# Optimization experiments

Hardware: AMD Instinct MI355X
Metric: run time of the kernel (lower is better)

Reference implementation:

```python
import jax, jax.numpy as jnp
import numpy as np

N_QUBITS = 8
EMBED_DIM = 1024
FFN_DIM = 4096


def _apply_1q_batched(state, gate, wire):
    # state: [N] + [2]*n ; gate: [N,2,2] (per-sample)
    n = state.ndim - 1
    N = state.shape[0]
    L = 2 ** wire
    R = 2 ** (n - 1 - wire)
    st = state.reshape(N, L, 2, R)
    st = jnp.einsum('nba,nlar->nlbr', gate, st)
    return st.reshape((N,) + (2,) * n)


def _apply_1q_shared(state, gate, wire):
    # gate: [2,2] shared across samples
    n = state.ndim - 1
    N = state.shape[0]
    L = 2 ** wire
    R = 2 ** (n - 1 - wire)
    st = state.reshape(N, L, 2, R)
    st = jnp.einsum('ba,nlar->nlbr', gate, st)
    return st.reshape((N,) + (2,) * n)


def _cnot(state, control, target):
    c_ax = control + 1
    t_ax = target + 1
    s0 = jnp.take(state, 0, axis=c_ax)
    s1 = jnp.take(state, 1, axis=c_ax)
    t_ax2 = t_ax - 1 if t_ax > c_ax else t_ax  # axis shift after take
    s1 = jnp.flip(s1, axis=t_ax2)
    return jnp.stack([s0, s1], axis=c_ax)


def _simulate(q_inputs, qparams):
    # q_inputs: [N, n_qubits] RX angles; qparams: [n_qubits, 3] Rot(phi,theta,omega)
    N = q_inputs.shape[0]
    n = N_QUBITS
    state = jnp.zeros((N, 2 ** n), dtype=jnp.complex64).at[:, 0].set(1.0)
    state = state.reshape((N,) + (2,) * n)
    # RX layer (per-sample angles)
    half = q_inputs.astype(jnp.float32) * 0.5
    c = jnp.cos(half).astype(jnp.complex64)
    s = (-1j) * jnp.sin(half).astype(jnp.complex64)
    for i in range(n):
        gate = jnp.stack([jnp.stack([c[:, i], s[:, i]], -1),
                          jnp.stack([s[:, i], c[:, i]], -1)], -2)  # [N,2,2]
        state = _apply_1q_batched(state, gate, i)
    # Rot layer: Rot(phi, theta, omega) = RZ(omega) RY(theta) RZ(phi)
    for i in range(n):
        phi, theta, omega = qparams[i, 0], qparams[i, 1], qparams[i, 2]
        ct = jnp.cos(theta / 2).astype(jnp.complex64)
        st = jnp.sin(theta / 2).astype(jnp.complex64)
        ep = jnp.exp(-0.5j * (phi + omega).astype(jnp.complex64))
        em = jnp.exp(0.5j * (phi - omega).astype(jnp.complex64))
        gate = jnp.array(0., jnp.complex64) + jnp.stack([
            jnp.stack([ep * ct, -em * st]),
            jnp.stack([jnp.conj(em) * st, jnp.conj(ep) * ct])])
        state = _apply_1q_shared(state, gate, i)
    # CNOT ring
    for i in range(n - 1):
        state = _cnot(state, i, i + 1)
    state = _cnot(state, n - 1, 0)
    # PauliZ expectations
    probs = jnp.abs(state) ** 2  # [N] + [2]*n, float32
    zs = []
    for i in range(n):
        axes = tuple(a for a in range(1, n + 1) if a != i + 1)
        m = probs.sum(axes)  # [N,2]
        zs.append(m[:, 0] - m[:, 1])
    return jnp.stack(zs, -1)  # [N, n_qubits]


def setup_inputs() -> dict:
    key = jax.random.key(0)
    k = jax.random.split(key, 6)
    x = jax.random.normal(k[0], (4, 2048, EMBED_DIM), dtype=jnp.float32)
    W1 = jax.random.normal(k[1], (FFN_DIM, EMBED_DIM), dtype=jnp.float32) * 0.02
    b1 = jnp.zeros((FFN_DIM,), dtype=jnp.float32)
    qparams = jax.random.normal(k[2], (N_QUBITS, 3), dtype=jnp.float32)
    W2 = jax.random.normal(k[3], (EMBED_DIM, N_QUBITS), dtype=jnp.float32) * 0.02
    b2 = jnp.zeros((EMBED_DIM,), dtype=jnp.float32)
    return {"x": x, "W1": W1, "b1": b1, "qparams": qparams, "W2": W2, "b2": b2}


def reference(x, W1, b1, qparams, W2, b2):
    batch, seq_len, embed_dim = x.shape
    x_flat = x.reshape(-1, embed_dim)
    x_ffn = x_flat @ W1.T + b1                       # [N, ffn_dim]
    q_inputs = x_ffn[:, :N_QUBITS]                   # ffn_dim >= n_qubits
    q_out = _simulate(q_inputs, qparams)             # [N, n_qubits]
    out = q_out @ W2.T + b2                          # [N, embed_dim]
    return out.reshape(batch, seq_len, embed_dim)
```

## Files before the change

kernel.cpp:

```cpp
#include <hip/hip_runtime.h>
#include <math.h>


constexpr int EMBED = 1024;
constexpr int NQ    = 8;
constexpr int BLOCK = 256;
constexpr int RPW   = 4;
constexpr int BR    = 16;
constexpr float INV2PI = 0.15915494309189535f;

__global__ __launch_bounds__(BLOCK, 2)
void ffq(const float* __restrict__ x,
         const float* __restrict__ W1,
         const float* __restrict__ b1,
         const float* __restrict__ qp,
         const float* __restrict__ W2,
         const float* __restrict__ b2,
         float* __restrict__ out,
         int total_rows)
{
    const int t    = threadIdx.x;
    const int lane = t & 63;
    const int wv   = t >> 6;
    const int j    = lane & 7;

    __shared__ float w1s[NQ * EMBED];
    __shared__ float w2t[NQ * EMBED];

    const long r0 = (long)blockIdx.x * BR + wv * RPW;

    float4 xv[RPW][4];
#pragma unroll
    for (int r = 0; r < RPW; ++r) {
        long row = r0 + r; if (row >= total_rows) row = total_rows - 1;
#pragma unroll
        for (int i = 0; i < 4; ++i)
            xv[r][i] = *reinterpret_cast<const float4*>(
                x + (size_t)row * EMBED + i * 256 + lane * 4);
    }

    {
        const float4* w1g = reinterpret_cast<const float4*>(W1);
        float4* w1d = reinterpret_cast<float4*>(w1s);
#pragma unroll
        for (int k = 0; k < (NQ * EMBED / 4) / BLOCK; ++k)
            w1d[k * BLOCK + t] = w1g[k * BLOCK + t];
#pragma unroll
        for (int m = 0; m < 4; ++m) {
            const int col = m * BLOCK + t;
            const float4 a = *reinterpret_cast<const float4*>(W2 + col * NQ);
            const float4 b = *reinterpret_cast<const float4*>(W2 + col * NQ + 4);
            w2t[0 * EMBED + col] = a.x;  w2t[1 * EMBED + col] = a.y;
            w2t[2 * EMBED + col] = a.z;  w2t[3 * EMBED + col] = a.w;
            w2t[4 * EMBED + col] = b.x;  w2t[5 * EMBED + col] = b.y;
            w2t[6 * EMBED + col] = b.z;  w2t[7 * EMBED + col] = b.w;
        }
    }

    float Rj, qoffj;
    {
        const float phi  = qp[j * 3 + 0];
        const float th   = qp[j * 3 + 1];
        const float cth  = cosf(th);
        const float ssps = sinf(th) * sinf(phi);
        Rj    = sqrtf(cth * cth + ssps * ssps);
        qoffj = (b1[j] + atan2f(ssps, cth)) * INV2PI;
    }

    float4 b2v[4];
#pragma unroll
    for (int i = 0; i < 4; ++i)
        b2v[i] = *reinterpret_cast<const float4*>(b2 + i * 256 + lane * 4);

    __syncthreads();

    float p[RPW][NQ];
#pragma unroll
    for (int r = 0; r < RPW; ++r)
#pragma unroll
        for (int jj = 0; jj < NQ; ++jj) p[r][jj] = 0.f;

#pragma unroll
    for (int i = 0; i < 4; ++i) {
#pragma unroll
        for (int jj = 0; jj < NQ; ++jj) {
            const float4 w = *reinterpret_cast<const float4*>(
                w1s + jj * EMBED + i * 256 + lane * 4);
#pragma unroll
            for (int r = 0; r < RPW; ++r) {
                p[r][jj] = fmaf(xv[r][i].x, w.x, p[r][jj]);
                p[r][jj] = fmaf(xv[r][i].y, w.y, p[r][jj]);
                p[r][jj] = fmaf(xv[r][i].z, w.z, p[r][jj]);
                p[r][jj] = fmaf(xv[r][i].w, w.w, p[r][jj]);
            }
        }
    }

    float qo[RPW][NQ];
#pragma unroll
    for (int r = 0; r < RPW; ++r) {
        float q4[4], q2[2], tsum;
        {
            const bool up = (lane & 4);
#pragma unroll
            for (int k = 0; k < 4; ++k) {
                const float snd = up ? p[r][k]     : p[r][k + 4];
                const float kp  = up ? p[r][k + 4] : p[r][k];
                q4[k] = kp + __shfl_xor(snd, 4, 64);
            }
        }
        {
            const bool up = (lane & 2);
#pragma unroll
            for (int k = 0; k < 2; ++k) {
                const float snd = up ? q4[k]     : q4[k + 2];
                const float kp  = up ? q4[k + 2] : q4[k];
                q2[k] = kp + __shfl_xor(snd, 2, 64);
            }
        }
        {
            const bool up = (lane & 1);
            const float snd = up ? q2[0] : q2[1];
            const float kp  = up ? q2[1] : q2[0];
            tsum = kp + __shfl_xor(snd, 1, 64);
        }
        tsum += __shfl_xor(tsum, 8, 64);
        tsum += __shfl_xor(tsum, 16, 64);
        tsum += __shfl_xor(tsum, 32, 64);

        const float zz = Rj * __builtin_amdgcn_cosf(tsum * INV2PI + qoffj);

        float z0_, z1_, z2_, z3_, z4_, z5_, z6_, z7_;
        {
            const float o  = __shfl_xor(zz, 1, 64);
            const float a0 = (lane & 1) ? o  : zz;
            const float a1 = (lane & 1) ? zz : o;
            const float rA = __shfl_xor(a0, 2, 64);
            const float rB = __shfl_xor(a1, 2, 64);
            const float c0 = (lane & 2) ? rA : a0;
            const float c1 = (lane & 2) ? rB : a1;
            const float c2 = (lane & 2) ? a0 : rA;
            const float c3 = (lane & 2) ? a1 : rB;
            const float d0 = __shfl_xor(c0, 4, 64);
            const float d1 = __shfl_xor(c1, 4, 64);
            const float d2 = __shfl_xor(c2, 4, 64);
            const float d3 = __shfl_xor(c3, 4, 64);
            z0_ = (lane & 4) ? d0 : c0;
            z1_ = (lane & 4) ? d1 : c1;
            z2_ = (lane & 4) ? d2 : c2;
            z3_ = (lane & 4) ? d3 : c3;
            z4_ = (lane & 4) ? c0 : d0;
            z5_ = (lane & 4) ? c1 : d1;
            z6_ = (lane & 4) ? c2 : d2;
            z7_ = (lane & 4) ? c3 : d3;
        }

        qo[r][1] = z0_ * z1_;
        qo[r][2] = qo[r][1] * z2_;
        qo[r][3] = qo[r][2] * z3_;
        qo[r][4] = qo[r][3] * z4_;
        qo[r][5] = qo[r][4] * z5_;
        qo[r][6] = qo[r][5] * z6_;
        qo[r][7] = qo[r][6] * z7_;
        qo[r][0] = z1_ * z2_ * z3_ * z4_ * z5_ * z6_ * z7_;
    }

#pragma unroll
    for (int i = 0; i < 4; ++i) {
        float4 w[NQ];
#pragma unroll
        for (int jj = 0; jj < NQ; ++jj)
            w[jj] = *reinterpret_cast<const float4*>(
                w2t + jj * EMBED + i * 256 + lane * 4);

#pragma unroll
        for (int r = 0; r < RPW; ++r) {
            const long row = r0 + r;
            if (row >= total_rows) continue;
            float4 o = b2v[i];
#pragma unroll
            for (int jj = 0; jj < NQ; ++jj) {
                o.x = fmaf(qo[r][jj], w[jj].x, o.x);
                o.y = fmaf(qo[r][jj], w[jj].y, o.y);
                o.z = fmaf(qo[r][jj], w[jj].z, o.z);
                o.w = fmaf(qo[r][jj], w[jj].w, o.w);
            }
            *reinterpret_cast<float4*>(
                out + (size_t)row * EMBED + i * 256 + lane * 4) = o;
        }
    }
}

extern "C" void kernel_launch(void* const* d_in, const int* in_sizes, int n_in,
                              void* d_out, int out_size, void* d_ws, size_t ws_size,
                              hipStream_t stream) {
    const float* x  = (const float*)d_in[0];
    const float* W1 = (const float*)d_in[1];
    const float* b1 = (const float*)d_in[2];
    const float* qp = (const float*)d_in[3];
    const float* W2 = (const float*)d_in[4];
    const float* b2 = (const float*)d_in[5];
    float* out = (float*)d_out;

    const int rows = in_sizes[0] / EMBED;
    const int grid = (rows + BR - 1) / BR;

    hipLaunchKernelGGL(ffq, dim3(grid), dim3(BLOCK), 0, stream,
                       x, W1, b1, qp, W2, b2, out, rows);
}
```

Before: 102.0 us.

## Keep W2 slice in registers and share qubit outputs via LDS across block rows

```diff
diff --git a/kernel.cpp b/kernel.cpp
--- a/kernel.cpp
+++ b/kernel.cpp
@@ -5,11 +5,11 @@
 constexpr int EMBED = 1024;
 constexpr int NQ    = 8;
 constexpr int BLOCK = 256;
-constexpr int RPW   = 4;
-constexpr int BR    = 16;
+constexpr int RPW   = 2;
+constexpr int BR    = 8;
 constexpr float INV2PI = 0.15915494309189535f;
 
-__global__ __launch_bounds__(BLOCK, 2)
+__global__ __launch_bounds__(BLOCK, 3)
 void ffq(const float* __restrict__ x,
          const float* __restrict__ W1,
          const float* __restrict__ b1,
@@ -25,37 +25,29 @@
     const int j    = lane & 7;
 
     __shared__ float w1s[NQ * EMBED];
-    __shared__ float w2t[NQ * EMBED];
-
-    const long r0 = (long)blockIdx.x * BR + wv * RPW;
+    __shared__ float qoS[BR][NQ];
+
+    const long blk0 = (long)blockIdx.x * BR;
+    const long r0w  = blk0 + wv * RPW;
 
     float4 xv[RPW][4];
 #pragma unroll
     for (int r = 0; r < RPW; ++r) {
-        long row = r0 + r; if (row >= total_rows) row = total_rows - 1;
+        long row = r0w + r; if (row >= total_rows) row = total_rows - 1;
 #pragma unroll
         for (int i = 0; i < 4; ++i)
             xv[r][i] = *reinterpret_cast<const float4*>(
                 x + (size_t)row * EMBED + i * 256 + lane * 4);
     }
 
-    {
-        const float4* w1g = reinterpret_cast<const float4*>(W1);
-        float4* w1d = reinterpret_cast<float4*>(w1s);
-#pragma unroll
-        for (int k = 0; k < (NQ * EMBED / 4) / BLOCK; ++k)
-            w1d[k * BLOCK + t] = w1g[k * BLOCK + t];
-#pragma unroll
-        for (int m = 0; m < 4; ++m) {
-            const int col = m * BLOCK + t;
-            const float4 a = *reinterpret_cast<const float4*>(W2 + col * NQ);
-            const float4 b = *reinterpret_cast<const float4*>(W2 + col * NQ + 4);
-            w2t[0 * EMBED + col] = a.x;  w2t[1 * EMBED + col] = a.y;
-            w2t[2 * EMBED + col] = a.z;  w2t[3 * EMBED + col] = a.w;
-            w2t[4 * EMBED + col] = b.x;  w2t[5 * EMBED + col] = b.y;
-            w2t[6 * EMBED + col] = b.z;  w2t[7 * EMBED + col] = b.w;
-        }
-    }
+    const int c = wv * 256 + lane * 4;
+    float4 wA[4], wB[4];
+#pragma unroll
+    for (int q = 0; q < 4; ++q) {
+        wA[q] = *reinterpret_cast<const float4*>(W2 + (c + q) * NQ);
+        wB[q] = *reinterpret_cast<const float4*>(W2 + (c + q) * NQ + 4);
+    }
+    const float4 bb = *reinterpret_cast<const float4*>(b2 + c);
 
     float Rj, qoffj;
     {
@@ -67,10 +59,13 @@
         qoffj = (b1[j] + atan2f(ssps, cth)) * INV2PI;
     }
 
-    float4 b2v[4];
-#pragma unroll
-    for (int i = 0; i < 4; ++i)
-        b2v[i] = *reinterpret_cast<const float4*>(b2 + i * 256 + lane * 4);
+    {
+        const float4* w1g = reinterpret_cast<const float4*>(W1);
+        float4* w1d = reinterpret_cast<float4*>(w1s);
+#pragma unroll
+        for (int k = 0; k < (NQ * EMBED / 4) / BLOCK; ++k)
+            w1d[k * BLOCK + t] = w1g[k * BLOCK + t];
+    }
 
     __syncthreads();
 
@@ -96,7 +91,6 @@
         }
     }
 
-    float qo[RPW][NQ];
 #pragma unroll
     for (int r = 0; r < RPW; ++r) {
         float q4[4], q2[2], tsum;
@@ -155,39 +149,49 @@
             z7_ = (lane & 4) ? c3 : d3;
         }
 
-        qo[r][1] = z0_ * z1_;
-        qo[r][2] = qo[r][1] * z2_;
-        qo[r][3] = qo[r][2] * z3_;
-        qo[r][4] = qo[r][3] * z4_;
-        qo[r][5] = qo[r][4] * z5_;
-        qo[r][6] = qo[r][5] * z6_;
-        qo[r][7] = qo[r][6] * z7_;
-        qo[r][0] = z1_ * z2_ * z3_ * z4_ * z5_ * z6_ * z7_;
-    }
-
-#pragma unroll
-    for (int i = 0; i < 4; ++i) {
-        float4 w[NQ];
-#pragma unroll
-        for (int jj = 0; jj < NQ; ++jj)
-            w[jj] = *reinterpret_cast<const float4*>(
-                w2t + jj * EMBED + i * 256 + lane * 4);
-
-#pragma unroll
-        for (int r = 0; r < RPW; ++r) {
-            const long row = r0 + r;
-            if (row >= total_rows) continue;
-            float4 o = b2v[i];
-#pragma unroll
-            for (int jj = 0; jj < NQ; ++jj) {
-                o.x = fmaf(qo[r][jj], w[jj].x, o.x);
-                o.y = fmaf(qo[r][jj], w[jj].y, o.y);
-                o.z = fmaf(qo[r][jj], w[jj].z, o.z);
-                o.w = fmaf(qo[r][jj], w[jj].w, o.w);
-            }
-            *reinterpret_cast<float4*>(
-                out + (size_t)row * EMBED + i * 256 + lane * 4) = o;
-        }
+        const float p1 = z0_ * z1_;
+        const float p2 = p1 * z2_;
+        const float p3 = p2 * z3_;
+        const float p4 = p3 * z4_;
+        const float p5 = p4 * z5_;
+        const float p6 = p5 * z6_;
+        const float p7 = p6 * z7_;
+        const float t7 = z1_ * z2_ * z3_ * z4_ * z5_ * z6_ * z7_;
+
+        float sel = p1;
+        sel = (j == 0) ? t7 : sel;
+        sel = (j == 2) ? p2 : sel;
+        sel = (j == 3) ? p3 : sel;
+        sel = (j == 4) ? p4 : sel;
+        sel = (j == 5) ? p5 : sel;
+        sel = (j == 6) ? p6 : sel;
+        sel = (j == 7) ? p7 : sel;
+
+        if (lane < NQ)
+            qoS[wv * RPW + r][lane] = sel;
+    }
+
+    __syncthreads();
+
+#pragma unroll
+    for (int r = 0; r < BR; ++r) {
+        const long row = blk0 + r;
+        if (row >= total_rows) break;
+
+        const float4 qA = *reinterpret_cast<const float4*>(&qoS[r][0]);
+        const float4 qB = *reinterpret_cast<const float4*>(&qoS[r][4]);
+
+        float4 o;
+        o.x = bb.x + qA.x*wA[0].x + qA.y*wA[0].y + qA.z*wA[0].z + qA.w*wA[0].w
+                   + qB.x*wB[0].x + qB.y*wB[0].y + qB.z*wB[0].z + qB.w*wB[0].w;
+        o.y = bb.y + qA.x*wA[1].x + qA.y*wA[1].y + qA.z*wA[1].z + qA.w*wA[1].w
+                   + qB.x*wB[1].x + qB.y*wB[1].y + qB.z*wB[1].z + qB.w*wB[1].w;
+        o.z = bb.z + qA.x*wA[2].x + qA.y*wA[2].y + qA.z*wA[2].z + qA.w*wA[2].w
+                   + qB.x*wB[2].x + qB.y*wB[2].y + qB.z*wB[2].z + qB.w*wB[2].w;
+        o.w = bb.w + qA.x*wA[3].x + qA.y*wA[3].y + qA.z*wA[3].z + qA.w*wA[3].w
+                   + qB.x*wB[3].x + qB.y*wB[3].y + qB.z*wB[3].z + qB.w*wB[3].w;
+
+        *reinterpret_cast<float4*>(out + (size_t)row * EMBED + c) = o;
     }
 }
 
```

After: 129.5 us. +27.0%, slower.

## Drop W2 LDS transpose, read W2 from global, halve rows per block, nontemporal stores

Applied to the files above, without the earlier changes.

```diff
diff --git a/kernel.cpp b/kernel.cpp
--- a/kernel.cpp
+++ b/kernel.cpp
@@ -5,11 +5,13 @@
 constexpr int EMBED = 1024;
 constexpr int NQ    = 8;
 constexpr int BLOCK = 256;
-constexpr int RPW   = 4;
-constexpr int BR    = 16;
+constexpr int RPW   = 2;
+constexpr int BR    = 8;
 constexpr float INV2PI = 0.15915494309189535f;
 
-__global__ __launch_bounds__(BLOCK, 2)
+using v4f = __attribute__((ext_vector_type(4))) float;
+
+__global__ __launch_bounds__(BLOCK, 3)
 void ffq(const float* __restrict__ x,
          const float* __restrict__ W1,
          const float* __restrict__ b1,
@@ -25,36 +27,18 @@
     const int j    = lane & 7;
 
     __shared__ float w1s[NQ * EMBED];
-    __shared__ float w2t[NQ * EMBED];
-
-    const long r0 = (long)blockIdx.x * BR + wv * RPW;
+
+    const long blk0 = (long)blockIdx.x * BR;
+    const long r0w  = blk0 + wv * RPW;
 
     float4 xv[RPW][4];
 #pragma unroll
     for (int r = 0; r < RPW; ++r) {
-        long row = r0 + r; if (row >= total_rows) row = total_rows - 1;
+        long row = r0w + r; if (row >= total_rows) row = total_rows - 1;
 #pragma unroll
         for (int i = 0; i < 4; ++i)
             xv[r][i] = *reinterpret_cast<const float4*>(
                 x + (size_t)row * EMBED + i * 256 + lane * 4);
-    }
-
-    {
-        const float4* w1g = reinterpret_cast<const float4*>(W1);
-        float4* w1d = reinterpret_cast<float4*>(w1s);
-#pragma unroll
-        for (int k = 0; k < (NQ * EMBED / 4) / BLOCK; ++k)
-            w1d[k * BLOCK + t] = w1g[k * BLOCK + t];
-#pragma unroll
-        for (int m = 0; m < 4; ++m) {
-            const int col = m * BLOCK + t;
-            const float4 a = *reinterpret_cast<const float4*>(W2 + col * NQ);
-            const float4 b = *reinterpret_cast<const float4*>(W2 + col * NQ + 4);
-            w2t[0 * EMBED + col] = a.x;  w2t[1 * EMBED + col] = a.y;
-            w2t[2 * EMBED + col] = a.z;  w2t[3 * EMBED + col] = a.w;
-            w2t[4 * EMBED + col] = b.x;  w2t[5 * EMBED + col] = b.y;
-            w2t[6 * EMBED + col] = b.z;  w2t[7 * EMBED + col] = b.w;
-        }
     }
 
     float Rj, qoffj;
@@ -67,10 +51,13 @@
         qoffj = (b1[j] + atan2f(ssps, cth)) * INV2PI;
     }
 
-    float4 b2v[4];
-#pragma unroll
-    for (int i = 0; i < 4; ++i)
-        b2v[i] = *reinterpret_cast<const float4*>(b2 + i * 256 + lane * 4);
+    {
+        const float4* w1g = reinterpret_cast<const float4*>(W1);
+        float4* w1d = reinterpret_cast<float4*>(w1s);
+#pragma unroll
+        for (int k = 0; k < (NQ * EMBED / 4) / BLOCK; ++k)
+            w1d[k * BLOCK + t] = w1g[k * BLOCK + t];
+    }
 
     __syncthreads();
 
@@ -166,27 +153,38 @@
     }
 
 #pragma unroll
-    for (int i = 0; i < 4; ++i) {
-        float4 w[NQ];
-#pragma unroll
-        for (int jj = 0; jj < NQ; ++jj)
-            w[jj] = *reinterpret_cast<const float4*>(
-                w2t + jj * EMBED + i * 256 + lane * 4);
-
-#pragma unroll
-        for (int r = 0; r < RPW; ++r) {
-            const long row = r0 + r;
-            if (row >= total_rows) continue;
-            float4 o = b2v[i];
-#pragma unroll
-            for (int jj = 0; jj < NQ; ++jj) {
-                o.x = fmaf(qo[r][jj], w[jj].x, o.x);
-                o.y = fmaf(qo[r][jj], w[jj].y, o.y);
-                o.z = fmaf(qo[r][jj], w[jj].z, o.z);
-                o.w = fmaf(qo[r][jj], w[jj].w, o.w);
-            }
-            *reinterpret_cast<float4*>(
-                out + (size_t)row * EMBED + i * 256 + lane * 4) = o;
+    for (int r = 0; r < RPW; ++r) {
+        const long row = r0w + r;
+        if (row >= total_rows) break;
+
+        const float q0 = qo[r][0], q1 = qo[r][1], q2_ = qo[r][2], q3 = qo[r][3];
+        const float q4_ = qo[r][4], q5 = qo[r][5], q6 = qo[r][6], q7 = qo[r][7];
+
+        float* outp = out + (size_t)row * EMBED;
+
+#pragma unroll
+        for (int i = 0; i < 4; ++i) {
+            const int c = i * 256 + lane * 4;
+
+            float4 wA[4], wB[4];
+#pragma unroll
+            for (int q = 0; q < 4; ++q) {
+                wA[q] = *reinterpret_cast<const float4*>(W2 + (c + q) * NQ);
+                wB[q] = *reinterpret_cast<const float4*>(W2 + (c + q) * NQ + 4);
+            }
+            const float4 bb = *reinterpret_cast<const float4*>(b2 + c);
+
+            v4f o;
+            o.x = bb.x + q0*wA[0].x + q1*wA[0].y + q2_*wA[0].z + q3*wA[0].w
+                       + q4_*wB[0].x + q5*wB[0].y + q6*wB[0].z + q7*wB[0].w;
+            o.y = bb.y + q0*wA[1].x + q1*wA[1].y + q2_*wA[1].z + q3*wA[1].w
+                       + q4_*wB[1].x + q5*wB[1].y + q6*wB[1].z + q7*wB[1].w;
+            o.z = bb.z + q0*wA[2].x + q1*wA[2].y + q2_*wA[2].z + q3*wA[2].w
+                       + q4_*wB[2].x + q5*wB[2].y + q6*wB[2].z + q7*wB[2].w;
+            o.w = bb.w + q0*wA[3].x + q1*wA[3].y + q2_*wA[3].z + q3*wA[3].w
+                       + q4_*wB[3].x + q5*wB[3].y + q6*wB[3].z + q7*wB[3].w;
+
+            __builtin_nontemporal_store(o, reinterpret_cast<v4f*>(outp + c));
         }
     }
 }
```

New measurement: 122.6 us. 20.2% more time.
